# Performance work log

Hardware: AMD Instinct MI355X
Metric: run time of the kernel (lower is better)

The kernel has to match this reference:

```python
import jax, jax.numpy as jnp
import numpy as np

A_FOCAL = 0.25
G_FOCAL = 2.0
SS_LOW = 0.4
SS_HIGH = 0.5
IOU_EPS = 0.01


def _xywh_to_xyxy(b):
    return jnp.concatenate([b[..., :2], b[..., :2] + b[..., 2:]], axis=-1)


def _focal(logits, t):
    # torchvision sigmoid_focal_loss, per-element
    p = jax.nn.sigmoid(logits)
    ce = -(t * jax.nn.log_sigmoid(logits) + (1.0 - t) * jax.nn.log_sigmoid(-logits))
    p_t = p * t + (1.0 - p) * (1.0 - t)
    a_t = A_FOCAL * t + (1.0 - A_FOCAL) * (1.0 - t)
    return a_t * ce * (1.0 - p_t) ** G_FOCAL


def setup_inputs() -> dict:
    key = jax.random.key(0)
    k1, k2, k3 = jax.random.split(key, 3)
    B, A, K = 4, 120000, 64
    ss_proposal = jax.random.uniform(k1, (B, A, 6), dtype=jnp.float32)
    anchors = jax.random.uniform(k2, (A, 4), dtype=jnp.float32)
    ground_truth = jax.random.uniform(k3, (B, K, 4), dtype=jnp.float32)
    return {"ss_proposal": ss_proposal, "anchors": anchors, "ground_truth": ground_truth}


def reference(ss_proposal, anchors, ground_truth):
    B = ss_proposal.shape[0]
    anc = _xywh_to_xyxy(anchors)              # (A,4) xyxy
    gt = _xywh_to_xyxy(ground_truth)          # (B,K,4) xyxy

    # pairwise IoU: (B, A, K)
    lt = jnp.maximum(anc[None, :, None, :2], gt[:, None, :, :2])
    rb = jnp.minimum(anc[None, :, None, 2:], gt[:, None, :, 2:])
    wh = jnp.clip(rb - lt, 0.0)
    inter = wh[..., 0] * wh[..., 1]
    area_a = (anc[:, 2] - anc[:, 0]) * (anc[:, 3] - anc[:, 1])        # (A,)
    area_g = (gt[..., 2] - gt[..., 0]) * (gt[..., 3] - gt[..., 1])    # (B,K)
    iou = inter / (area_a[None, :, None] + area_g[:, None, :] - inter)

    best = jnp.argmax(iou, axis=-1)           # (B,A)
    target_score = jnp.max(iou, axis=-1)      # (B,A)
    # target boxes in xywh (code converts back before gather)
    target_boxes = jnp.take_along_axis(ground_truth, best[:, :, None], axis=1)  # (B,A,4)

    logits = ss_proposal[..., 4]              # (B,A)
    pos = target_score >= SS_HIGH
    neg = target_score < SS_LOW
    pos_count = jnp.sum(pos, axis=-1).astype(jnp.float32)             # (B,)

    stc_sum = (jnp.sum(jnp.where(pos, _focal(logits, 1.0), 0.0), axis=-1)
               + jnp.sum(jnp.where(neg, _focal(logits, 0.0), 0.0), axis=-1))
    safe = jnp.where(pos_count > 0, pos_count, 1.0)
    stc = stc_sum / safe                      # undivided sum if pos_count==0 (safe==1)

    # elementwise IoU of predicted boxes vs matched targets (diagonal of box_iou)
    pb = _xywh_to_xyxy(ss_proposal[..., :4])  # (B,A,4)
    tb = _xywh_to_xyxy(target_boxes)          # (B,A,4)
    elt = jnp.maximum(pb[..., :2], tb[..., :2])
    erb = jnp.minimum(pb[..., 2:], tb[..., 2:])
    ewh = jnp.clip(erb - elt, 0.0)
    einter = ewh[..., 0] * ewh[..., 1]
    pa = (pb[..., 2] - pb[..., 0]) * (pb[..., 3] - pb[..., 1])
    ta = (tb[..., 2] - tb[..., 0]) * (tb[..., 3] - tb[..., 1])
    eiou = einter / (pa + ta - einter)
    iou_l = -jnp.log(eiou + IOU_EPS)
    str_sum = jnp.sum(jnp.where(pos, iou_l, 0.0), axis=-1)
    str_loss = jnp.where(pos_count > 0, str_sum / safe, 0.0)

    total = (jnp.sum(stc) + jnp.sum(str_loss)) / B
    return total
```

## Files before the change

kernel.cpp:

```cpp
#include <hip/hip_runtime.h>
#include <cmath>

#define BLOCK 1024
#define APT 2
#define CH 8

__global__ void __launch_bounds__(BLOCK) ainno_main(
    const float* __restrict__ ss,
    const float* __restrict__ anchors,
    const float* __restrict__ gt,
    float* __restrict__ part,
    int A, int K, int B)
{
    __shared__ float4 gxy_s[64];
    __shared__ float  gar_s[64];
    __shared__ float  red[(BLOCK / 64) * 3];

    const int b    = blockIdx.y;
    const int tid  = threadIdx.x;
    const int lane = tid & 63;

    if (tid < K) {
        float4 g = ((const float4*)(gt + (size_t)b * K * 4))[tid];
        float x2 = g.x + g.z, y2 = g.y + g.w;
        gxy_s[tid] = make_float4(g.x, g.y, x2, y2);
        gar_s[tid] = (x2 - g.x) * (y2 - g.y);
    }
    __syncthreads();

    const int tileSz = BLOCK * APT;
    const int ntiles = (A + tileSz - 1) / tileSz;

    float posf = 0.f, stcs = 0.f, strs = 0.f;

    for (int tt = blockIdx.x; tt < ntiles; tt += gridDim.x) {
        const int base = tt * tileSz + tid;

        float ax[APT], ay[APT], axx[APT], ayy[APT], aar[APT];
        float bi[APT], bd[APT];
        int   bk[APT];
        #pragma unroll
        for (int i = 0; i < APT; ++i) {
            int a  = base + i * BLOCK;
            int ac = a < A ? a : A - 1;
            float4 an = ((const float4*)anchors)[ac];
            ax[i]  = an.x;         ay[i]  = an.y;
            axx[i] = an.x + an.z;  ayy[i] = an.y + an.w;
            aar[i] = (axx[i] - ax[i]) * (ayy[i] - ay[i]);
            bi[i] = -1.f; bd[i] = 1.f; bk[i] = 0;
        }

        const int kfull = K & ~(CH - 1);
        for (int k0 = 0; k0 < kfull; k0 += CH) {
            float4 gg[CH];
            float  sar[CH];
            #pragma unroll
            for (int j = 0; j < CH; ++j) {
                gg[j]  = gxy_s[k0 + j];
                sar[j] = gar_s[k0 + j];
            }
            #pragma unroll
            for (int j = 0; j < CH; ++j) {
                #pragma unroll
                for (int i = 0; i < APT; ++i) {
                    float w = fminf(axx[i], gg[j].z) - fmaxf(ax[i], gg[j].x);
                    float h = fminf(ayy[i], gg[j].w) - fmaxf(ay[i], gg[j].y);
                    w = fmaxf(w, 0.f); h = fmaxf(h, 0.f);
                    float inter = w * h;
                    float S = aar[i] + sar[j];
                    bool better = inter * bd[i] > bi[i] * S;
                    bi[i] = better ? inter : bi[i];
                    bd[i] = better ? S     : bd[i];
                    bk[i] = better ? (k0 + j) : bk[i];
                }
            }
        }
        for (int k = kfull; k < K; ++k) {
            float4 gg  = gxy_s[k];
            float  sar = gar_s[k];
            #pragma unroll
            for (int i = 0; i < APT; ++i) {
                float w = fminf(axx[i], gg.z) - fmaxf(ax[i], gg.x);
                float h = fminf(ayy[i], gg.w) - fmaxf(ay[i], gg.y);
                w = fmaxf(w, 0.f); h = fmaxf(h, 0.f);
                float inter = w * h;
                float S = aar[i] + sar;
                bool better = inter * bd[i] > bi[i] * S;
                bi[i] = better ? inter : bi[i];
                bd[i] = better ? S     : bd[i];
                bk[i] = better ? k     : bk[i];
            }
        }

        #pragma unroll
        for (int i = 0; i < APT; ++i) {
            int a = base + i * BLOCK;
            float4 wb  = gxy_s[bk[i]];
            float  war = gar_s[bk[i]];

            float score = bi[i] / (bd[i] - bi[i]);
            bool inb = a < A;
            bool pos = inb && (score >= 0.5f);
            bool neg = inb && (score < 0.4f);
            if (pos | neg) {
                const float* sp = ss + ((size_t)b * A + a) * 6;
                float x = sp[4];
                float e = expf(-x);
                float p = 1.f / (1.f + e);
                if (pos) {
                    posf += 1.f;
                    float ce  = log1pf(e);
                    float omp = 1.f - p;
                    stcs += 0.25f * ce * omp * omp;

                    float px  = sp[0], py = sp[1];
                    float pxx = px + sp[2], pyy = py + sp[3];
                    float ew = fminf(pxx, wb.z) - fmaxf(px, wb.x);
                    float eh = fminf(pyy, wb.w) - fmaxf(py, wb.y);
                    ew = fmaxf(ew, 0.f); eh = fmaxf(eh, 0.f);
                    float einter = ew * eh;
                    float pa = (pxx - px) * (pyy - py);
                    float eiou = einter / (pa + war - einter);
                    strs += -logf(eiou + 0.01f);
                } else {
                    float ce = log1pf(expf(x));
                    stcs += 0.75f * ce * p * p;
                }
            }
        }
    }

    float v0 = posf, v1 = stcs, v2 = strs;
    for (int off = 32; off > 0; off >>= 1) {
        v0 += __shfl_down(v0, off, 64);
        v1 += __shfl_down(v1, off, 64);
        v2 += __shfl_down(v2, off, 64);
    }
    const int wave = tid >> 6;
    if (lane == 0) {
        red[wave * 3 + 0] = v0;
        red[wave * 3 + 1] = v1;
        red[wave * 3 + 2] = v2;
    }
    __syncthreads();
    if (tid == 0) {
        float s0 = 0.f, s1 = 0.f, s2 = 0.f;
        for (int w = 0; w < BLOCK / 64; ++w) {
            s0 += red[w * 3 + 0];
            s1 += red[w * 3 + 1];
            s2 += red[w * 3 + 2];
        }
        ((float4*)part)[(size_t)b * gridDim.x + blockIdx.x] =
            make_float4(s0, s1, s2, 0.f);
    }
}

__global__ void ainno_final(const float* __restrict__ part,
                            float* __restrict__ out, int GX, int B)
{
    __shared__ float tot_s[4];
    const int tid = threadIdx.x, lane = tid & 63, wave = tid >> 6;
    float t = 0.f;
    for (int bb = wave; bb < B; bb += 4) {
        float pc = 0.f, st = 0.f, sr = 0.f;
        for (int i = lane; i < GX; i += 64) {
            const float* p = part + ((size_t)bb * GX + i) * 4;
            pc += p[0]; st += p[1]; sr += p[2];
        }
        for (int off = 32; off > 0; off >>= 1) {
            pc += __shfl_down(pc, off, 64);
            st += __shfl_down(st, off, 64);
            sr += __shfl_down(sr, off, 64);
        }
        if (lane == 0) {
            float safe = pc > 0.f ? pc : 1.f;
            float v = st / safe;
            if (pc > 0.f) v += sr / safe;
            t += v;
        }
    }
    if (lane == 0) tot_s[wave] = t;
    __syncthreads();
    if (tid == 0) {
        float s = 0.f;
        for (int w = 0; w < 4; ++w) s += tot_s[w];
        out[0] = s / (float)B;
    }
}

extern "C" void kernel_launch(void* const* d_in, const int* in_sizes, int n_in,
                              void* d_out, int out_size, void* d_ws, size_t ws_size,
                              hipStream_t stream) {
    const float* ss      = (const float*)d_in[0];
    const float* anchors = (const float*)d_in[1];
    const float* gt      = (const float*)d_in[2];
    float* out  = (float*)d_out;
    float* part = (float*)d_ws;

    const int A = in_sizes[1] / 4;
    const int B = in_sizes[0] / (A * 6);
    const int K = in_sizes[2] / (B * 4);

    const int tileSz = BLOCK * APT;
    const int ntiles = (A + tileSz - 1) / tileSz;
    const int gx     = ntiles;

    dim3 grid(gx, B);
    ainno_main<<<grid, BLOCK, 0, stream>>>(ss, anchors, gt, part, A, K, B);
    ainno_final<<<dim3(1), 256, 0, stream>>>(part, out, gx, B);
}
```

Before: 84.34 us.

## Double-buffer GT LDS reads, recompute GT areas, prefetch logits before argmax

Specializes the K==64 path with a two-buffer software pipeline over the ground-truth boxes in LDS, using sched_barrier so the next chunk's LDS loads are issued while the current chunk is consumed. GT areas are now recomputed from the cached corners instead of read from a separate shared array, which trades LDS traffic for a few ALU ops. The logit load from global memory is hoisted ahead of the IoU loop so its latency overlaps the compute. The cost is higher register pressure at BLOCK=1024 and an unconditional global load even for anchors that end up ignored.

```diff
diff --git a/kernel.cpp b/kernel.cpp
--- a/kernel.cpp
+++ b/kernel.cpp
@@ -4,6 +4,35 @@
 #define BLOCK 1024
 #define APT 2
 #define CH 8
+
+struct ArgmaxState {
+    float bi[APT], bd[APT];
+    int   bk[APT];
+};
+
+__device__ __forceinline__ void consume_chunk(
+    const float4* __restrict__ buf, int kbase,
+    const float* ax, const float* ay, const float* axx, const float* ayy,
+    const float* aar, ArgmaxState& st)
+{
+    #pragma unroll
+    for (int j = 0; j < CH; ++j) {
+        float4 g = buf[j];
+        float sar = (g.z - g.x) * (g.w - g.y);
+        #pragma unroll
+        for (int i = 0; i < APT; ++i) {
+            float w = fminf(axx[i], g.z) - fmaxf(ax[i], g.x);
+            float h = fminf(ayy[i], g.w) - fmaxf(ay[i], g.y);
+            w = fmaxf(w, 0.f); h = fmaxf(h, 0.f);
+            float inter = w * h;
+            float S = aar[i] + sar;
+            bool better = inter * st.bd[i] > st.bi[i] * S;
+            st.bi[i] = better ? inter : st.bi[i];
+            st.bd[i] = better ? S     : st.bd[i];
+            st.bk[i] = better ? kbase + j : st.bk[i];
+        }
+    }
+}
 
 __global__ void __launch_bounds__(BLOCK) ainno_main(
     const float* __restrict__ ss,
@@ -13,7 +42,6 @@
     int A, int K, int B)
 {
     __shared__ float4 gxy_s[64];
-    __shared__ float  gar_s[64];
     __shared__ float  red[(BLOCK / 64) * 3];
 
     const int b    = blockIdx.y;
@@ -22,9 +50,7 @@
 
     if (tid < K) {
         float4 g = ((const float4*)(gt + (size_t)b * K * 4))[tid];
-        float x2 = g.x + g.z, y2 = g.y + g.w;
-        gxy_s[tid] = make_float4(g.x, g.y, x2, y2);
-        gar_s[tid] = (x2 - g.x) * (y2 - g.y);
+        gxy_s[tid] = make_float4(g.x, g.y, g.x + g.z, g.y + g.w);
     }
     __syncthreads();
 
@@ -37,8 +63,7 @@
         const int base = tt * tileSz + tid;
 
         float ax[APT], ay[APT], axx[APT], ayy[APT], aar[APT];
-        float bi[APT], bd[APT];
-        int   bk[APT];
+        ArgmaxState st;
         #pragma unroll
         for (int i = 0; i < APT; ++i) {
             int a  = base + i * BLOCK;
@@ -47,64 +72,63 @@
             ax[i]  = an.x;         ay[i]  = an.y;
             axx[i] = an.x + an.z;  ayy[i] = an.y + an.w;
             aar[i] = (axx[i] - ax[i]) * (ayy[i] - ay[i]);
-            bi[i] = -1.f; bd[i] = 1.f; bk[i] = 0;
-        }
-
-        const int kfull = K & ~(CH - 1);
-        for (int k0 = 0; k0 < kfull; k0 += CH) {
-            float4 gg[CH];
-            float  sar[CH];
+            st.bi[i] = -1.f; st.bd[i] = 1.f; st.bk[i] = 0;
+        }
+
+        const float* sp0 = ss + ((size_t)b * A + (base         < A ? base         : A - 1)) * 6;
+        const float* sp1 = ss + ((size_t)b * A + (base + BLOCK < A ? base + BLOCK : A - 1)) * 6;
+        float xlog0 = sp0[4];
+        float xlog1 = sp1[4];
+
+        if (K == 64) {
+            float4 bufA[CH], bufB[CH];
             #pragma unroll
-            for (int j = 0; j < CH; ++j) {
-                gg[j]  = gxy_s[k0 + j];
-                sar[j] = gar_s[k0 + j];
+            for (int j = 0; j < CH; ++j) bufA[j] = gxy_s[j];
+            #pragma unroll 1
+            for (int k0 = 0; k0 < 64; k0 += 2 * CH) {
+                #pragma unroll
+                for (int j = 0; j < CH; ++j) bufB[j] = gxy_s[k0 + CH + j];
+                __builtin_amdgcn_sched_barrier(0);
+                consume_chunk(bufA, k0, ax, ay, axx, ayy, aar, st);
+                if (k0 + 2 * CH < 64) {
+                    #pragma unroll
+                    for (int j = 0; j < CH; ++j) bufA[j] = gxy_s[k0 + 2 * CH + j];
+                }
+                __builtin_amdgcn_sched_barrier(0);
+                consume_chunk(bufB, k0 + CH, ax, ay, axx, ayy, aar, st);
             }
-            #pragma unroll
-            for (int j = 0; j < CH; ++j) {
+        } else {
+            for (int k = 0; k < K; ++k) {
+                float4 g = gxy_s[k];
+                float sar = (g.z - g.x) * (g.w - g.y);
                 #pragma unroll
                 for (int i = 0; i < APT; ++i) {
-                    float w = fminf(axx[i], gg[j].z) - fmaxf(ax[i], gg[j].x);
-                    float h = fminf(ayy[i], gg[j].w) - fmaxf(ay[i], gg[j].y);
+                    float w = fminf(axx[i], g.z) - fmaxf(ax[i], g.x);
+                    float h = fminf(ayy[i], g.w) - fmaxf(ay[i], g.y);
                     w = fmaxf(w, 0.f); h = fmaxf(h, 0.f);
                     float inter = w * h;
-                    float S = aar[i] + sar[j];
-                    bool better = inter * bd[i] > bi[i] * S;
-                    bi[i] = better ? inter : bi[i];
-                    bd[i] = better ? S     : bd[i];
-                    bk[i] = better ? (k0 + j) : bk[i];
+                    float S = aar[i] + sar;
+                    bool better = inter * st.bd[i] > st.bi[i] * S;
+                    st.bi[i] = better ? inter : st.bi[i];
+                    st.bd[i] = better ? S     : st.bd[i];
+                    st.bk[i] = better ? k     : st.bk[i];
                 }
-            }
-        }
-        for (int k = kfull; k < K; ++k) {
-            float4 gg  = gxy_s[k];
-            float  sar = gar_s[k];
-            #pragma unroll
-            for (int i = 0; i < APT; ++i) {
-                float w = fminf(axx[i], gg.z) - fmaxf(ax[i], gg.x);
-                float h = fminf(ayy[i], gg.w) - fmaxf(ay[i], gg.y);
-                w = fmaxf(w, 0.f); h = fmaxf(h, 0.f);
-                float inter = w * h;
-                float S = aar[i] + sar;
-                bool better = inter * bd[i] > bi[i] * S;
-                bi[i] = better ? inter : bi[i];
-                bd[i] = better ? S     : bd[i];
-                bk[i] = better ? k     : bk[i];
             }
         }
 
         #pragma unroll
         for (int i = 0; i < APT; ++i) {
             int a = base + i * BLOCK;
-            float4 wb  = gxy_s[bk[i]];
-            float  war = gar_s[bk[i]];
-
-            float score = bi[i] / (bd[i] - bi[i]);
+            float4 wb  = gxy_s[st.bk[i]];
+            float  war = (wb.z - wb.x) * (wb.w - wb.y);
+
+            float score = st.bi[i] / (st.bd[i] - st.bi[i]);
             bool inb = a < A;
             bool pos = inb && (score >= 0.5f);
             bool neg = inb && (score < 0.4f);
             if (pos | neg) {
-                const float* sp = ss + ((size_t)b * A + a) * 6;
-                float x = sp[4];
+                const float* sp = (i == 0) ? sp0 : sp1;
+                float x = (i == 0) ? xlog0 : xlog1;
                 float e = expf(-x);
                 float p = 1.f / (1.f + e);
                 if (pos) {
```

Result: slower. 100.1 us (+18.7%).
